# Kernel optimization log

Measured on AMD Instinct MI355X. Metric: run time of the kernel, lower is better.

The kernel has to match this reference:

```python
import jax, jax.numpy as jnp
import numpy as np
from jax import lax

DN = ('NCHW', 'OIHW', 'NCHW')

def conv(x, w, b, stride):
    y = lax.conv_general_dilated(x, w, (stride, stride), ((1, 1), (1, 1)), dimension_numbers=DN)
    return y + b[None, :, None, None]

def deconv(x, w, b):
    # PyTorch ConvTranspose2d(k=3, stride=2, padding=1, output_padding=1): doubles H, W.
    # w has torch layout [in, out, kH, kW]; convert to OIHW and flip spatially.
    wt = jnp.flip(w, (-2, -1)).transpose(1, 0, 2, 3)
    y = lax.conv_general_dilated(x, wt, (1, 1), ((1, 2), (1, 2)), lhs_dilation=(2, 2), dimension_numbers=DN)
    return y + b[None, :, None, None]


def setup_inputs() -> dict:
    key = jax.random.key(0)
    ks = jax.random.split(key, 16)
    s = 0.05
    d = {
        'x': jax.random.normal(ks[0], (16, 3, 256, 256), jnp.float32),
        'w1': jax.random.normal(ks[1], (64, 3, 3, 3), jnp.float32) * s,
        'b1': jnp.zeros((64,), jnp.float32),
        'w2': jax.random.normal(ks[2], (128, 64, 3, 3), jnp.float32) * s,
        'b2': jnp.zeros((128,), jnp.float32),
        'w3': jax.random.normal(ks[3], (256, 128, 3, 3), jnp.float32) * s,
        'b3': jnp.zeros((256,), jnp.float32),
        'w4': jax.random.normal(ks[4], (512, 256, 3, 3), jnp.float32) * s,
        'b4': jnp.zeros((512,), jnp.float32),
        'codebook': jax.random.normal(ks[5], (8192, 512), jnp.float32),
        # ConvTranspose2d weights in torch layout [in, out, kH, kW]
        'd1w': jax.random.normal(ks[6], (512, 256, 3, 3), jnp.float32) * s,
        'd1b': jnp.zeros((256,), jnp.float32),
        'd2w': jax.random.normal(ks[7], (256, 128, 3, 3), jnp.float32) * s,
        'd2b': jnp.zeros((128,), jnp.float32),
        'd3w': jax.random.normal(ks[8], (128, 64, 3, 3), jnp.float32) * s,
        'd3b': jnp.zeros((64,), jnp.float32),
        'wo': jax.random.normal(ks[9], (3, 64, 3, 3), jnp.float32) * s,
        'bo': jnp.zeros((3,), jnp.float32),
    }
    return d


def reference(x, w1, b1, w2, b2, w3, b3, w4, b4, codebook, d1w, d1b, d2w, d2b, d3w, d3b, wo, bo):
    # Encoder: 256 -> 256 -> 128 -> 64 -> 32 spatial
    h = jax.nn.relu(conv(x, w1, b1, 1))
    h = jax.nn.relu(conv(h, w2, b2, 2))
    h = jax.nn.relu(conv(h, w3, b3, 2))
    z = conv(h, w4, b4, 2)  # [B, 512, 32, 32]

    # Quantize: nearest codebook entry per spatial vector (channels-last).
    B, C, H, W = z.shape
    zf = z.transpose(0, 2, 3, 1).reshape(-1, C)  # [N, 512]
    # squared euclidean distances; argmin identical to cdist argmin
    d2 = (jnp.sum(zf * zf, axis=-1, keepdims=True)
          - 2.0 * (zf @ codebook.T)
          + jnp.sum(codebook * codebook, axis=-1))  # [N, K]
    indices = jnp.argmin(d2, axis=-1)  # [N]
    zq = codebook[indices].reshape(B, H, W, C).transpose(0, 3, 1, 2)  # [B, 512, 32, 32]

    # Decoder: 32 -> 64 -> 128 -> 256
    g = jax.nn.relu(deconv(zq, d1w, d1b))
    g = jax.nn.relu(deconv(g, d2w, d2b))
    g = jax.nn.relu(deconv(g, d3w, d3b))
    x_recon = jax.nn.sigmoid(conv(g, wo, bo, 1))
    return x_recon, indices
```

## Files before the change

kernel.cpp:

```cpp
#include <hip/hip_runtime.h>
#include <cstddef>

typedef short short8 __attribute__((ext_vector_type(8)));
typedef _Float16 half8 __attribute__((ext_vector_type(8)));
typedef _Float16 half4 __attribute__((ext_vector_type(4)));
typedef _Float16 half2v __attribute__((ext_vector_type(2)));
typedef float floatx4 __attribute__((ext_vector_type(4)));

__device__ __forceinline__ unsigned short f2bf(float f) {
    unsigned u = __float_as_uint(f);
    u += 0x7FFFu + ((u >> 16) & 1u);
    return (unsigned short)(u >> 16);
}
__device__ __forceinline__ float bf2f(unsigned short h) {
    return __uint_as_float((unsigned)h << 16);
}

__global__ __launch_bounds__(256)
void fused_conv12_mfma_kernel(const float* __restrict__ x,
                              const float* __restrict__ w1,
                              const float* __restrict__ b1,
                              const _Float16* __restrict__ w2h,
                              const _Float16* __restrict__ w2l,
                              const float* __restrict__ b2,
                              _Float16* __restrict__ outH,
                              _Float16* __restrict__ outL)
{
    __shared__ float s_x[3][11][36];
    __shared__ _Float16 sE[2][9][17][40];
    __shared__ _Float16 sO[2][9][16][40];

    const int tid = threadIdx.x;
    const int lane = tid & 63;
    const int wave = tid >> 6;
    const int n16 = lane & 15;
    const int quad = lane >> 4;

    const int ox0 = (blockIdx.x & 7) * 16;
    const int oy0 = (blockIdx.x >> 3) * 4;
    const int co0 = blockIdx.y * 64 + wave * 16;
    const int img = blockIdx.z;

    const int hy0 = oy0 * 2 - 1, hx0 = ox0 * 2 - 1;
    const int gy0 = hy0 - 1,     gx0 = hx0 - 1;
    const float* xN = x + (size_t)img * 3 * 65536;

    for (int e = tid; e < 3 * 11 * 35; e += 256) {
        int c = e / 385, r = e % 385;
        int yy = r / 35, xx = r % 35;
        int gy = gy0 + yy, gx = gx0 + xx;
        float v = 0.f;
        if ((unsigned)gy < 256u && (unsigned)gx < 256u)
            v = xN[(size_t)c * 65536 + gy * 256 + gx];
        s_x[c][yy][xx] = v;
    }

    floatx4 acc1[4], acc2[4];
#pragma unroll
    for (int s = 0; s < 4; s++) {
        acc1[s] = (floatx4){0.f, 0.f, 0.f, 0.f};
        acc2[s] = (floatx4){0.f, 0.f, 0.f, 0.f};
    }

    const int pair = tid & 15;
    const int pxg  = tid >> 4;

    for (int c0 = 0; c0 < 64; c0 += 32) {
        __syncthreads();

        const int ch0 = c0 + pair * 2;
        float wA[27], wB[27];
#pragma unroll
        for (int k = 0; k < 27; k++) {
            wA[k] = w1[ch0 * 27 + k];
            wB[k] = w1[ch0 * 27 + 27 + k];
        }
        const float bA = b1[ch0], bB = b1[ch0 + 1];

        for (int px = pxg; px < 33; px += 16) {
            const bool colok = (unsigned)(hx0 + px) < 256u;
            float xw[3][3][3];
#pragma unroll
            for (int c = 0; c < 3; c++)
#pragma unroll
                for (int r = 0; r < 3; r++)
#pragma unroll
                    for (int kx = 0; kx < 3; kx++)
                        xw[c][r][kx] = s_x[c][r][px + kx];
#pragma unroll
            for (int py = 0; py < 9; py++) {
                const bool inb = colok && (unsigned)(hy0 + py) < 256u;
                float aA = bA, aB = bB;
#pragma unroll
                for (int c = 0; c < 3; c++)
#pragma unroll
                    for (int k = 0; k < 9; k++) {
                        const float xv = xw[c][k / 3][k % 3];
                        aA += wA[c * 9 + k] * xv;
                        aB += wB[c * 9 + k] * xv;
                    }
                float vA = inb ? fmaxf(aA, 0.f) : 0.f;
                float vB = inb ? fmaxf(aB, 0.f) : 0.f;
                half2v hv, lv;
                _Float16 hA = (_Float16)vA, hB = (_Float16)vB;
                hv[0] = hA; hv[1] = hB;
                lv[0] = (_Float16)((vA - (float)hA) * 1024.f);
                lv[1] = (_Float16)((vB - (float)hB) * 1024.f);
                _Float16* dH = (px & 1) ? &sO[0][py][px >> 1][pair * 2]
                                        : &sE[0][py][px >> 1][pair * 2];
                _Float16* dL = (px & 1) ? &sO[1][py][px >> 1][pair * 2]
                                        : &sE[1][py][px >> 1][pair * 2];
                *(half2v*)dH = hv;
                *(half2v*)dL = lv;
                if (py < 8) {
#pragma unroll
                    for (int c = 0; c < 3; c++) {
#pragma unroll
                        for (int r = 0; r < 2; r++)
#pragma unroll
                            for (int kx = 0; kx < 3; kx++)
                                xw[c][r][kx] = xw[c][r + 1][kx];
#pragma unroll
                        for (int kx = 0; kx < 3; kx++)
                            xw[c][2][kx] = s_x[c][py + 3][px + kx];
                    }
                }
            }
        }
        __syncthreads();

        half8 ah[9], al[9];
#pragma unroll
        for (int tp = 0; tp < 9; tp++) {
            size_t o = ((size_t)(tp * 128 + co0 + n16)) * 64 + c0 + quad * 8;
            ah[tp] = *(const half8*)(w2h + o);
            al[tp] = *(const half8*)(w2l + o);
        }
#pragma unroll
        for (int oy = 0; oy < 4; oy++) {
#pragma unroll
            for (int tp = 0; tp < 9; tp++) {
                const int kx = tp % 3;
                const int row = oy * 2 + tp / 3;
                half8 bh, bl;
                if (kx == 0)      { bh = *(const half8*)&sE[0][row][n16][quad * 8];
                                    bl = *(const half8*)&sE[1][row][n16][quad * 8]; }
                else if (kx == 1) { bh = *(const half8*)&sO[0][row][n16][quad * 8];
                                    bl = *(const half8*)&sO[1][row][n16][quad * 8]; }
                else              { bh = *(const half8*)&sE[0][row][n16 + 1][quad * 8];
                                    bl = *(const half8*)&sE[1][row][n16 + 1][quad * 8]; }
                acc1[oy] = __builtin_amdgcn_mfma_f32_16x16x32_f16(ah[tp], bh, acc1[oy], 0, 0, 0);
                acc2[oy] = __builtin_amdgcn_mfma_f32_16x16x32_f16(ah[tp], bl, acc2[oy], 0, 0, 0);
                acc2[oy] = __builtin_amdgcn_mfma_f32_16x16x32_f16(al[tp], bh, acc2[oy], 0, 0, 0);
            }
        }
    }

    const float4 bv = *(const float4*)&b2[co0 + quad * 4];
    const float bb[4] = {bv.x, bv.y, bv.z, bv.w};
#pragma unroll
    for (int oy = 0; oy < 4; oy++) {
        half4 hv, lv;
#pragma unroll
        for (int r = 0; r < 4; r++) {
            float v = fmaxf(acc1[oy][r] + acc2[oy][r] * (1.0f / 1024.0f) + bb[r], 0.f);
            _Float16 h = (_Float16)v;
            hv[r] = h;
            lv[r] = (_Float16)((v - (float)h) * 1024.f);
        }
        size_t o = (((size_t)img * 128 + (oy0 + oy)) * 128 + (ox0 + n16)) * 128
                   + co0 + quad * 4;
        *(half4*)(outH + o) = hv;
        *(half4*)(outL + o) = lv;
    }
}

template<int CI, int CO>
__global__ __launch_bounds__(256)
void prepack_conv_kernel(const float* __restrict__ w,
                         _Float16* __restrict__ wh, _Float16* __restrict__ wl)
{
    int i = blockIdx.x * 256 + threadIdx.x;
    if (i >= CO * CI * 9) return;
    int co = i / (CI * 9);
    int r  = i % (CI * 9);
    int ci = r / 9;
    int tp = r % 9;
    float v = w[i];
    _Float16 h = (_Float16)v;
    size_t o = ((size_t)tp * CO + co) * CI + ci;
    wh[o] = h;
    wl[o] = (_Float16)((v - (float)h) * 1024.f);
}

template<int CIN, int COUT, int IH, int IW, bool RELU>
__global__ __launch_bounds__(256)
void conv_mfma_kernel(const _Float16* __restrict__ inH, const _Float16* __restrict__ inL,
                      const _Float16* __restrict__ wpH, const _Float16* __restrict__ wpL,
                      const float* __restrict__ bias,
                      _Float16* __restrict__ outH, _Float16* __restrict__ outL)
{
    constexpr int OH = IH / 2, OW = IW / 2;
    __shared__ _Float16 sE[2][9][17][40];
    __shared__ _Float16 sO[2][9][16][40];

    const int tid = threadIdx.x;
    const int lane = tid & 63;
    const int wave = tid >> 6;
    const int n16 = lane & 15;
    const int quad = lane >> 4;

    constexpr int NTX = OW / 16;
    const int ox0 = (blockIdx.x % NTX) * 16;
    const int oy0 = (blockIdx.x / NTX) * 4;
    const int co0 = blockIdx.y * 64 + wave * 16;
    const int img = blockIdx.z;

    const int iy0 = oy0 * 2 - 1;
    const int ix0 = ox0 * 2 - 1;
    const _Float16* iNH = inH + (size_t)img * IH * IW * CIN;
    const _Float16* iNL = inL + (size_t)img * IH * IW * CIN;

    floatx4 acc1[4], acc2[4];
#pragma unroll
    for (int s = 0; s < 4; s++) {
        acc1[s] = (floatx4){0.f, 0.f, 0.f, 0.f};
        acc2[s] = (floatx4){0.f, 0.f, 0.f, 0.f};
    }

    for (int k0 = 0; k0 < CIN; k0 += 32) {
        __syncthreads();
        for (int e = tid; e < 2376; e += 256) {
            int pl = e / 1188;
            int r  = e % 1188;
            int pix = r >> 2, q = r & 3;
            int py = pix / 33, px = pix % 33;
            int iy = iy0 + py, ix = ix0 + px;
            half8 v = (half8)(_Float16)0;
            if ((unsigned)iy < (unsigned)IH && (unsigned)ix < (unsigned)IW)
                v = *(const half8*)((pl ? iNL : iNH) + ((size_t)(iy * IW + ix) * CIN + k0 + q * 8));
            if (px & 1) *(half8*)&sO[pl][py][px >> 1][q * 8] = v;
            else        *(half8*)&sE[pl][py][px >> 1][q * 8] = v;
        }
        __syncthreads();

        half8 ah[9], al[9];
#pragma unroll
        for (int tp = 0; tp < 9; tp++) {
            size_t o = ((size_t)(tp * COUT + co0 + n16)) * CIN + k0 + quad * 8;
            ah[tp] = *(const half8*)(wpH + o);
            al[tp] = *(const half8*)(wpL + o);
        }

#pragma unroll
        for (int oy = 0; oy < 4; oy++) {
#pragma unroll
            for (int tp = 0; tp < 9; tp++) {
                const int ky = tp / 3, kx = tp % 3;
                const int row = oy * 2 + ky;
                half8 bh, bl;
                if (kx == 0)      { bh = *(const half8*)&sE[0][row][n16][quad * 8];
                                    bl = *(const half8*)&sE[1][row][n16][quad * 8]; }
                else if (kx == 1) { bh = *(const half8*)&sO[0][row][n16][quad * 8];
                                    bl = *(const half8*)&sO[1][row][n16][quad * 8]; }
                else              { bh = *(const half8*)&sE[0][row][n16 + 1][quad * 8];
                                    bl = *(const half8*)&sE[1][row][n16 + 1][quad * 8]; }
                acc1[oy] = __builtin_amdgcn_mfma_f32_16x16x32_f16(ah[tp], bh, acc1[oy], 0, 0, 0);
                acc2[oy] = __builtin_amdgcn_mfma_f32_16x16x32_f16(ah[tp], bl, acc2[oy], 0, 0, 0);
                acc2[oy] = __builtin_amdgcn_mfma_f32_16x16x32_f16(al[tp], bh, acc2[oy], 0, 0, 0);
            }
        }
    }

    const float4 bv = *(const float4*)&bias[co0 + quad * 4];
    const float bb[4] = {bv.x, bv.y, bv.z, bv.w};
#pragma unroll
    for (int oy = 0; oy < 4; oy++) {
        half4 hv, lv;
#pragma unroll
        for (int r = 0; r < 4; r++) {
            float v = acc1[oy][r] + acc2[oy][r] * (1.0f / 1024.0f) + bb[r];
            if (RELU) v = fmaxf(v, 0.f);
            _Float16 h = (_Float16)v;
            hv[r] = h;
            lv[r] = (_Float16)((v - (float)h) * 1024.f);
        }
        size_t o = (((size_t)img * OH + (oy0 + oy)) * OW + (ox0 + n16)) * COUT
                   + co0 + quad * 4;
        *(half4*)(outH + o) = hv;
        *(half4*)(outL + o) = lv;
    }
}

__global__ __launch_bounds__(64)
void cnorm_kernel(const float* __restrict__ cb, float* __restrict__ cn)
{
    const int code = blockIdx.x;
    const int t = threadIdx.x;
    const float* row = cb + (size_t)code * 512;
    float s = 0.f;
    for (int i = t; i < 512; i += 64) s += row[i] * row[i];
#pragma unroll
    for (int off = 32; off > 0; off >>= 1) s += __shfl_down(s, off, 64);
    if (t == 0) cn[code] = s;
}

__global__ __launch_bounds__(256)
void init_keys_kernel(unsigned long long* __restrict__ keys)
{
    keys[blockIdx.x * 256 + threadIdx.x] = ~0ull;
}

__global__ __launch_bounds__(256)
void split_cb_kernel(const float* __restrict__ cb,
                     _Float16* __restrict__ ch, _Float16* __restrict__ cl)
{
    size_t i = (size_t)blockIdx.x * 256 + threadIdx.x;
    float v = cb[i];
    _Float16 h = (_Float16)v;
    ch[i] = h;
    cl[i] = (_Float16)((v - (float)h) * 1024.f);
}

__global__ __launch_bounds__(256)
void vq_mfma_kernel(const _Float16* __restrict__ zh, const _Float16* __restrict__ zl,
                    const _Float16* __restrict__ ch, const _Float16* __restrict__ cl,
                    const float* __restrict__ cn,
                    unsigned long long* __restrict__ keys)
{
    __shared__ _Float16 sB[2][2][128][40];

    const int tid = threadIdx.x;
    const int lane = tid & 63;
    const int wave = tid >> 6;
    const int n16 = lane & 15;
    const int quad = lane >> 4;

    const int row0 = blockIdx.x * 128 + wave * 32;
    const int code0 = blockIdx.y * 128;

    floatx4 acc1[2][8], acc2[2][8];
#pragma unroll
    for (int rt = 0; rt < 2; rt++)
#pragma unroll
        for (int ct = 0; ct < 8; ct++) {
            acc1[rt][ct] = (floatx4){0.f, 0.f, 0.f, 0.f};
            acc2[rt][ct] = (floatx4){0.f, 0.f, 0.f, 0.f};
        }

    const _Float16* pzh = zh + (size_t)(row0 + n16) * 512 + quad * 8;
    const _Float16* pzl = zl + (size_t)(row0 + n16) * 512 + quad * 8;

    half8 As[2][4];
    As[0][0] = *(const half8*)(pzh);
    As[0][1] = *(const half8*)(pzh + 8192);
    As[0][2] = *(const half8*)(pzl);
    As[0][3] = *(const half8*)(pzl + 8192);
#pragma unroll
    for (int it = 0; it < 4; ++it) {
        int e = tid + it * 256;
        int pl = e >> 9, r = (e >> 2) & 127, q = e & 3;
        const _Float16* src = (pl ? cl : ch) + (size_t)(code0 + r) * 512 + q * 8;
        *(half8*)&sB[0][pl][r][q * 8] = *(const half8*)src;
    }
    __syncthreads();

#pragma unroll 2
    for (int c = 0; c < 16; ++c) {
        const int cur = c & 1;
        if (c < 15) {
            const int nxt = cur ^ 1;
            const int kk = (c + 1) * 32;
            As[nxt][0] = *(const half8*)(pzh + kk);
            As[nxt][1] = *(const half8*)(pzh + 8192 + kk);
            As[nxt][2] = *(const half8*)(pzl + kk);
            As[nxt][3] = *(const half8*)(pzl + 8192 + kk);
#pragma unroll
            for (int it = 0; it < 4; ++it) {
                int e = tid + it * 256;
                int pl = e >> 9, r = (e >> 2) & 127, q = e & 3;
                const _Float16* src = (pl ? cl : ch) + (size_t)(code0 + r) * 512 + kk + q * 8;
                *(half8*)&sB[nxt][pl][r][q * 8] = *(const half8*)src;
            }
        }
#pragma unroll
        for (int ct = 0; ct < 8; ++ct) {
            half8 bh = *(const half8*)&sB[cur][0][ct * 16 + n16][quad * 8];
            half8 bl = *(const half8*)&sB[cur][1][ct * 16 + n16][quad * 8];
            acc1[0][ct] = __builtin_amdgcn_mfma_f32_16x16x32_f16(As[cur][0], bh, acc1[0][ct], 0, 0, 0);
            acc1[1][ct] = __builtin_amdgcn_mfma_f32_16x16x32_f16(As[cur][1], bh, acc1[1][ct], 0, 0, 0);
            acc2[0][ct] = __builtin_amdgcn_mfma_f32_16x16x32_f16(As[cur][0], bl, acc2[0][ct], 0, 0, 0);
            acc2[1][ct] = __builtin_amdgcn_mfma_f32_16x16x32_f16(As[cur][1], bl, acc2[1][ct], 0, 0, 0);
            acc2[0][ct] = __builtin_amdgcn_mfma_f32_16x16x32_f16(As[cur][2], bh, acc2[0][ct], 0, 0, 0);
            acc2[1][ct] = __builtin_amdgcn_mfma_f32_16x16x32_f16(As[cur][3], bh, acc2[1][ct], 0, 0, 0);
        }
        __syncthreads();
    }

#pragma unroll
    for (int rt = 0; rt < 2; rt++) {
#pragma unroll
        for (int reg = 0; reg < 4; reg++) {
            float best = 3.0e38f;
            int bcode = 0;
#pragma unroll
            for (int ct = 0; ct < 8; ct++) {
                const int code = code0 + ct * 16 + n16;
                float dot = acc1[rt][ct][reg] + acc2[rt][ct][reg] * (1.0f / 1024.0f);
                float s = cn[code] - 2.0f * dot;
                if (s < best) { best = s; bcode = code; }
            }
            unsigned u = __float_as_uint(best);
            u = (u & 0x80000000u) ? ~u : (u | 0x80000000u);
            unsigned long long key = ((unsigned long long)u << 32) | (unsigned)bcode;
#pragma unroll
            for (int m = 1; m < 16; m <<= 1) {
                unsigned long long o = __shfl_xor(key, m, 64);
                key = (o < key) ? o : key;
            }
            if (n16 == 0)
                atomicMin(&keys[row0 + rt * 16 + quad * 4 + reg], key);
        }
    }
}

__global__ __launch_bounds__(256)
void vq_gather_kernel(const unsigned long long* __restrict__ keys,
                      const float* __restrict__ cb,
                      unsigned short* __restrict__ zq, float* __restrict__ idx_out)
{
    __shared__ int sidx[64];
    const int t = threadIdx.x;
    const int v0 = blockIdx.x * 64;
    if (t < 64) {
        int idx = (int)(keys[v0 + t] & 0xFFFFFFFFull);
        sidx[t] = idx;
        idx_out[v0 + t] = (float)idx;
    }
    __syncthreads();
    const int tv = t >> 2;
    const int q = t & 3;
    const float* crow = cb + (size_t)sidx[tv] * 512;
    unsigned short* zrow = zq + (size_t)(v0 + tv) * 512;
    for (int c = q * 8; c < 512; c += 32) {
        float4 f0 = *(const float4*)(crow + c);
        float4 f1 = *(const float4*)(crow + c + 4);
        short8 h;
        h[0] = (short)f2bf(f0.x); h[1] = (short)f2bf(f0.y);
        h[2] = (short)f2bf(f0.z); h[3] = (short)f2bf(f0.w);
        h[4] = (short)f2bf(f1.x); h[5] = (short)f2bf(f1.y);
        h[6] = (short)f2bf(f1.z); h[7] = (short)f2bf(f1.w);
        *(short8*)(zrow + c) = h;
    }
}

template<int CI, int CO>
__global__ __launch_bounds__(256)
void prepack_kernel(const float* __restrict__ w, unsigned short* __restrict__ wp)
{
    int i = blockIdx.x * 256 + threadIdx.x;
    if (i >= 9 * CO * CI) return;
    int ci = i / (CO * 9);
    int r  = i % (CO * 9);
    int co = r / 9;
    int tp = r % 9;
    wp[((size_t)tp * CO + co) * CI + ci] = f2bf(w[i]);
}

template<int CIN, int COUT, int IH, int IW, bool OUT_NCHW>
__global__ __launch_bounds__(256)
void deconv_mfma_kernel(const unsigned short* __restrict__ in,
                        const unsigned short* __restrict__ wp,
                        const float* __restrict__ bias,
                        unsigned short* __restrict__ out)
{
    constexpr int OH = 2 * IH, OW = 2 * IW;
    __shared__ short sIn[5][17][40];

    const int tid = threadIdx.x;
    const int lane = tid & 63;
    const int wave = tid >> 6;
    const int n16 = lane & 15;
    const int quad = lane >> 4;

    constexpr int NTX = IW / 16;
    const int x0 = (blockIdx.x % NTX) * 16;
    const int y0 = (blockIdx.x / NTX) * 4;
    const int co0 = blockIdx.y * 64 + wave * 16;
    const int img = blockIdx.z;

    const unsigned short* inN = in + (size_t)img * IH * IW * CIN;

    floatx4 acc[4][4];
#pragma unroll
    for (int s = 0; s < 4; s++)
#pragma unroll
        for (int c = 0; c < 4; c++) acc[s][c] = (floatx4){0.f, 0.f, 0.f, 0.f};

    for (int k0 = 0; k0 < CIN; k0 += 32) {
        __syncthreads();
        for (int e = tid; e < 340; e += 256) {
            int yy = e / 68, r = e % 68;
            int xx = r >> 2, q4 = r & 3;
            int gy = y0 + yy, gx = x0 + xx;
            short8 v = {0, 0, 0, 0, 0, 0, 0, 0};
            if (gy < IH && gx < IW)
                v = *(const short8*)(inN + ((size_t)(gy * IW + gx) * CIN + k0 + q4 * 8));
            *(short8*)&sIn[yy][xx][q4 * 8] = v;
        }
        __syncthreads();

        short8 a[9];
#pragma unroll
        for (int tp = 0; tp < 9; tp++)
            a[tp] = *(const short8*)(wp + ((size_t)(tp * COUT + co0 + n16) * CIN + k0 + quad * 8));

#pragma unroll
        for (int s = 0; s < 4; s++) {
            short8 b00 = *(const short8*)&sIn[s    ][n16    ][quad * 8];
            short8 b01 = *(const short8*)&sIn[s    ][n16 + 1][quad * 8];
            short8 b10 = *(const short8*)&sIn[s + 1][n16    ][quad * 8];
            short8 b11 = *(const short8*)&sIn[s + 1][n16 + 1][quad * 8];
            acc[s][0] = __builtin_amdgcn_mfma_f32_16x16x32_bf16(a[4], b00, acc[s][0], 0, 0, 0);
            acc[s][1] = __builtin_amdgcn_mfma_f32_16x16x32_bf16(a[3], b01, acc[s][1], 0, 0, 0);
            acc[s][1] = __builtin_amdgcn_mfma_f32_16x16x32_bf16(a[5], b00, acc[s][1], 0, 0, 0);
            acc[s][2] = __builtin_amdgcn_mfma_f32_16x16x32_bf16(a[1], b10, acc[s][2], 0, 0, 0);
            acc[s][2] = __builtin_amdgcn_mfma_f32_16x16x32_bf16(a[7], b00, acc[s][2], 0, 0, 0);
            acc[s][3] = __builtin_amdgcn_mfma_f32_16x16x32_bf16(a[0], b11, acc[s][3], 0, 0, 0);
            acc[s][3] = __builtin_amdgcn_mfma_f32_16x16x32_bf16(a[2], b10, acc[s][3], 0, 0, 0);
            acc[s][3] = __builtin_amdgcn_mfma_f32_16x16x32_bf16(a[6], b01, acc[s][3], 0, 0, 0);
            acc[s][3] = __builtin_amdgcn_mfma_f32_16x16x32_bf16(a[8], b00, acc[s][3], 0, 0, 0);
        }
    }

    const float4 bv = *(const float4*)&bias[co0 + quad * 4];
    const float bb[4] = {bv.x, bv.y, bv.z, bv.w};
    const int x = x0 + n16;

    if (!OUT_NCHW) {
        unsigned short* outN = out + (size_t)img * OH * OW * COUT;
#pragma unroll
        for (int s = 0; s < 4; s++) {
            const int y = y0 + s;
#pragma unroll
            for (int c = 0; c < 4; c++) {
                const int oy = 2 * y + (c >> 1);
                const int ox = 2 * x + (c & 1);
                ushort4 h;
                h.x = f2bf(fmaxf(acc[s][c][0] + bb[0], 0.f));
                h.y = f2bf(fmaxf(acc[s][c][1] + bb[1], 0.f));
                h.z = f2bf(fmaxf(acc[s][c][2] + bb[2], 0.f));
                h.w = f2bf(fmaxf(acc[s][c][3] + bb[3], 0.f));
                *(ushort4*)(outN + ((size_t)(oy * OW + ox) * COUT + co0 + quad * 4)) = h;
            }
        }
    } else {
#pragma unroll
        for (int s = 0; s < 4; s++) {
            const int y = y0 + s;
#pragma unroll
            for (int r = 0; r < 4; r++) {
                const int co = co0 + quad * 4 + r;
                unsigned short* oC = out + (size_t)(img * COUT + co) * OH * OW;
                unsigned p0 = (unsigned)f2bf(fmaxf(acc[s][0][r] + bb[r], 0.f)) |
                              ((unsigned)f2bf(fmaxf(acc[s][1][r] + bb[r], 0.f)) << 16);
                unsigned p1 = (unsigned)f2bf(fmaxf(acc[s][2][r] + bb[r], 0.f)) |
                              ((unsigned)f2bf(fmaxf(acc[s][3][r] + bb[r], 0.f)) << 16);
                *(unsigned*)(oC + (size_t)(2 * y) * OW + 2 * x) = p0;
                *(unsigned*)(oC + (size_t)(2 * y + 1) * OW + 2 * x) = p1;
            }
        }
    }
}

__global__ __launch_bounds__(256)
void conv_out_kernel(const unsigned short* __restrict__ in,
                     const float* __restrict__ w,
                     const float* __restrict__ bias,
                     float* __restrict__ out)
{
    constexpr int TIC = 4;
    __shared__ float s_in[TIC][3][258];
    const int t = threadIdx.x;
    const int y = blockIdx.x;
    const int n = blockIdx.y;
    const unsigned short* inN = in + (size_t)n * 64 * 65536;
    float acc0 = bias[0], acc1 = bias[1], acc2 = bias[2];

    for (int c0 = 0; c0 < 64; c0 += TIC) {
        for (int e = t; e < TIC * 3 * 258; e += 256) {
            int ci = e / 774;
            int r  = e % 774;
            int ry = r / 258, xx = r % 258;
            int gy = y - 1 + ry, gx = xx - 1;
            float v = 0.f;
            if ((unsigned)gy < 256u && (unsigned)gx < 256u)
                v = bf2f(inN[(size_t)(c0 + ci) * 65536 + gy * 256 + gx]);
            s_in[ci][ry][xx] = v;
        }
        __syncthreads();
#pragma unroll
        for (int ci = 0; ci < TIC; ++ci) {
            float iv[3][3];
#pragma unroll
            for (int ry = 0; ry < 3; ry++)
#pragma unroll
                for (int kx = 0; kx < 3; kx++)
                    iv[ry][kx] = s_in[ci][ry][t + kx];
#pragma unroll
            for (int k = 0; k < 9; k++) {
                const float v = iv[k / 3][k % 3];
                acc0 += w[(0 * 64 + c0 + ci) * 9 + k] * v;
                acc1 += w[(1 * 64 + c0 + ci) * 9 + k] * v;
                acc2 += w[(2 * 64 + c0 + ci) * 9 + k] * v;
            }
        }
        __syncthreads();
    }
    const size_t o = (size_t)((n * 3 + 0) * 256 + y) * 256 + t;
    out[o]          = 1.f / (1.f + __expf(-acc0));
    out[o + 65536]  = 1.f / (1.f + __expf(-acc1));
    out[o + 131072] = 1.f / (1.f + __expf(-acc2));
}

extern "C" void kernel_launch(void* const* d_in, const int* in_sizes, int n_in,
                              void* d_out, int out_size, void* d_ws, size_t ws_size,
                              hipStream_t stream)
{
    const float* x   = (const float*)d_in[0];
    const float* w1  = (const float*)d_in[1];
    const float* b1  = (const float*)d_in[2];
    const float* w2  = (const float*)d_in[3];
    const float* b2  = (const float*)d_in[4];
    const float* w3  = (const float*)d_in[5];
    const float* b3  = (const float*)d_in[6];
    const float* w4  = (const float*)d_in[7];
    const float* b4  = (const float*)d_in[8];
    const float* cb  = (const float*)d_in[9];
    const float* d1w = (const float*)d_in[10];
    const float* d1b = (const float*)d_in[11];
    const float* d2w = (const float*)d_in[12];
    const float* d2b = (const float*)d_in[13];
    const float* d3w = (const float*)d_in[14];
    const float* d3b = (const float*)d_in[15];
    const float* wo  = (const float*)d_in[16];
    const float* bo  = (const float*)d_in[17];

    char* ws = (char*)d_ws;
    _Float16* H2H = (_Float16*)(ws);
    _Float16* H2L = (_Float16*)(ws + 67108864);
    _Float16* H3H = (_Float16*)(ws + 134217728);
    _Float16* H3L = (_Float16*)(ws + 167772160);
    _Float16* ZH  = (_Float16*)(ws);
    _Float16* ZL  = (_Float16*)(ws + 16777216);
    unsigned short* ZQ = (unsigned short*)(ws + 33554432);
    _Float16* CBH = (_Float16*)(ws + 50331648);
    _Float16* CBL = (_Float16*)(ws + 58720256);
    unsigned short* G1 = (unsigned short*)(ws + 67108864);
    unsigned short* G2 = (unsigned short*)(ws + 134217728);
    unsigned short* G3 = (unsigned short*)(ws);
    unsigned long long* keys = (unsigned long long*)(ws + 201326592);
    float* cn = (float*)(ws + 201326592 + 131072);

    char* oscratch = (char*)d_out;
    _Float16* EW3H = (_Float16*)(oscratch);
    _Float16* EW3L = (_Float16*)(oscratch + 589824);
    _Float16* EW4H = (_Float16*)(oscratch + 1179648);
    _Float16* EW4L = (_Float16*)(oscratch + 3538944);
    unsigned short* WP1 = (unsigned short*)(oscratch + 5898240);
    unsigned short* WP2 = (unsigned short*)(oscratch + 8257536);
    unsigned short* WP3 = (unsigned short*)(oscratch + 8847360);
    _Float16* EW2H = (_Float16*)(oscratch + 8994816);
    _Float16* EW2L = (_Float16*)(oscratch + 9142272);

    float* xrec = (float*)d_out;
    float* idxf = (float*)d_out + (size_t)16 * 3 * 256 * 256;

    prepack_conv_kernel<64,  128><<<288,  256, 0, stream>>>(w2, EW2H, EW2L);
    prepack_conv_kernel<128, 256><<<1152, 256, 0, stream>>>(w3, EW3H, EW3L);
    prepack_conv_kernel<256, 512><<<4608, 256, 0, stream>>>(w4, EW4H, EW4L);
    prepack_kernel<512, 256><<<4608, 256, 0, stream>>>(d1w, WP1);
    prepack_kernel<256, 128><<<1152, 256, 0, stream>>>(d2w, WP2);
    prepack_kernel<128, 64 ><<<288,  256, 0, stream>>>(d3w, WP3);

    fused_conv12_mfma_kernel<<<dim3(256, 2, 16), 256, 0, stream>>>(x, w1, b1, EW2H, EW2L, b2, H2H, H2L);
    conv_mfma_kernel<128, 256, 128, 128, true ><<<dim3(64, 4, 16), 256, 0, stream>>>(H2H, H2L, EW3H, EW3L, b3, H3H, H3L);
    conv_mfma_kernel<256, 512, 64,  64,  false><<<dim3(16, 8, 16), 256, 0, stream>>>(H3H, H3L, EW4H, EW4L, b4, ZH, ZL);

    cnorm_kernel<<<8192, 64, 0, stream>>>(cb, cn);
    init_keys_kernel<<<64, 256, 0, stream>>>(keys);
    split_cb_kernel<<<16384, 256, 0, stream>>>(cb, CBH, CBL);
    vq_mfma_kernel<<<dim3(128, 64), 256, 0, stream>>>(ZH, ZL, CBH, CBL, cn, keys);
    vq_gather_kernel<<<256, 256, 0, stream>>>(keys, cb, ZQ, idxf);

    deconv_mfma_kernel<512, 256, 32,  32,  false><<<dim3(16,  4, 16), 256, 0, stream>>>(ZQ, WP1, d1b, G1);
    deconv_mfma_kernel<256, 128, 64,  64,  false><<<dim3(64,  2, 16), 256, 0, stream>>>(G1, WP2, d2b, G2);
    deconv_mfma_kernel<128, 64,  128, 128, true ><<<dim3(256, 1, 16), 256, 0, stream>>>(G2, WP3, d3b, G3);
    conv_out_kernel<<<dim3(256, 16), 256, 0, stream>>>(G3, wo, bo, xrec);
}
```

Before: 2.332 ms.

## Retile VQ distance kernel to 256 rows x 64 codes per block

Changes the VQ MFMA kernel tiling from 128 rows x 128 codes to 256 rows x 64 codes per block, with each wave computing a 64x64 tile (4x4 MFMA tiles). The codebook tile in shared memory is laid out linearly so each lane's fragment is contiguous, dropping the padded 2D layout. Next-chunk codebook loads are issued into registers before the MFMAs and stored to shared memory afterwards, giving a register-staged prefetch. The intent is better reuse of the loaded codebook fragments and fewer shared-memory reads per MFMA. The grid mapping changes (blockIdx.x now indexes codes), so the launch site must match, and the linear layout may cause LDS bank conflicts.

```diff
diff --git a/kernel.cpp b/kernel.cpp
--- a/kernel.cpp
+++ b/kernel.cpp
@@ -328,7 +328,7 @@
                     const float* __restrict__ cn,
                     unsigned long long* __restrict__ keys)
 {
-    __shared__ _Float16 sB[2][2][128][40];
+    __shared__ _Float16 sB[2][512 * 8];
 
     const int tid = threadIdx.x;
     const int lane = tid & 63;
@@ -336,14 +336,14 @@
     const int n16 = lane & 15;
     const int quad = lane >> 4;
 
-    const int row0 = blockIdx.x * 128 + wave * 32;
-    const int code0 = blockIdx.y * 128;
-
-    floatx4 acc1[2][8], acc2[2][8];
-#pragma unroll
-    for (int rt = 0; rt < 2; rt++)
-#pragma unroll
-        for (int ct = 0; ct < 8; ct++) {
+    const int code0 = blockIdx.x * 64;
+    const int row0 = blockIdx.y * 256 + wave * 64;
+
+    floatx4 acc1[4][4], acc2[4][4];
+#pragma unroll
+    for (int rt = 0; rt < 4; rt++)
+#pragma unroll
+        for (int ct = 0; ct < 4; ct++) {
             acc1[rt][ct] = (floatx4){0.f, 0.f, 0.f, 0.f};
             acc2[rt][ct] = (floatx4){0.f, 0.f, 0.f, 0.f};
         }
@@ -351,60 +351,57 @@
     const _Float16* pzh = zh + (size_t)(row0 + n16) * 512 + quad * 8;
     const _Float16* pzl = zl + (size_t)(row0 + n16) * 512 + quad * 8;
 
-    half8 As[2][4];
-    As[0][0] = *(const half8*)(pzh);
-    As[0][1] = *(const half8*)(pzh + 8192);
-    As[0][2] = *(const half8*)(pzl);
-    As[0][3] = *(const half8*)(pzl + 8192);
-#pragma unroll
-    for (int it = 0; it < 4; ++it) {
-        int e = tid + it * 256;
-        int pl = e >> 9, r = (e >> 2) & 127, q = e & 3;
-        const _Float16* src = (pl ? cl : ch) + (size_t)(code0 + r) * 512 + q * 8;
-        *(half8*)&sB[0][pl][r][q * 8] = *(const half8*)src;
-    }
+    const int e0 = tid, e1 = tid + 256;
+    const _Float16* s0 = ((e0 >> 8) ? cl : ch)
+        + (size_t)(code0 + ((e0 >> 6) & 3) * 16 + ((e0 >> 2) & 15)) * 512 + (e0 & 3) * 8;
+    const _Float16* s1 = ((e1 >> 8) ? cl : ch)
+        + (size_t)(code0 + ((e1 >> 6) & 3) * 16 + ((e1 >> 2) & 15)) * 512 + (e1 & 3) * 8;
+
+    *(half8*)&sB[0][e0 * 8] = *(const half8*)s0;
+    *(half8*)&sB[0][e1 * 8] = *(const half8*)s1;
     __syncthreads();
 
-#pragma unroll 2
     for (int c = 0; c < 16; ++c) {
         const int cur = c & 1;
+        const int kk = c * 32;
+        half8 ah[4], al[4];
+#pragma unroll
+        for (int rt = 0; rt < 4; rt++) {
+            ah[rt] = *(const half8*)(pzh + (size_t)rt * 8192 + kk);
+            al[rt] = *(const half8*)(pzl + (size_t)rt * 8192 + kk);
+        }
+        half8 t0, t1;
+        if (c < 15) {
+            t0 = *(const half8*)(s0 + kk + 32);
+            t1 = *(const half8*)(s1 + kk + 32);
+        }
+#pragma unroll
+        for (int ct = 0; ct < 4; ++ct) {
+            half8 bh = *(const half8*)&sB[cur][(ct * 64 + n16 * 4 + quad) * 8];
+            half8 bl = *(const half8*)&sB[cur][(256 + ct * 64 + n16 * 4 + quad) * 8];
+#pragma unroll
+            for (int rt = 0; rt < 4; rt++) {
+                acc1[rt][ct] = __builtin_amdgcn_mfma_f32_16x16x32_f16(ah[rt], bh, acc1[rt][ct], 0, 0, 0);
+                acc2[rt][ct] = __builtin_amdgcn_mfma_f32_16x16x32_f16(ah[rt], bl, acc2[rt][ct], 0, 0, 0);
+                acc2[rt][ct] = __builtin_amdgcn_mfma_f32_16x16x32_f16(al[rt], bh, acc2[rt][ct], 0, 0, 0);
+            }
+        }
         if (c < 15) {
             const int nxt = cur ^ 1;
-            const int kk = (c + 1) * 32;
-            As[nxt][0] = *(const half8*)(pzh + kk);
-            As[nxt][1] = *(const half8*)(pzh + 8192 + kk);
-            As[nxt][2] = *(const half8*)(pzl + kk);
-            As[nxt][3] = *(const half8*)(pzl + 8192 + kk);
-#pragma unroll
-            for (int it = 0; it < 4; ++it) {
-                int e = tid + it * 256;
-                int pl = e >> 9, r = (e >> 2) & 127, q = e & 3;
-                const _Float16* src = (pl ? cl : ch) + (size_t)(code0 + r) * 512 + kk + q * 8;
-                *(half8*)&sB[nxt][pl][r][q * 8] = *(const half8*)src;
-            }
-        }
-#pragma unroll
-        for (int ct = 0; ct < 8; ++ct) {
-            half8 bh = *(const half8*)&sB[cur][0][ct * 16 + n16][quad * 8];
-            half8 bl = *(const half8*)&sB[cur][1][ct * 16 + n16][quad * 8];
-            acc1[0][ct] = __builtin_amdgcn_mfma_f32_16x16x32_f16(As[cur][0], bh, acc1[0][ct], 0, 0, 0);
-            acc1[1][ct] = __builtin_amdgcn_mfma_f32_16x16x32_f16(As[cur][1], bh, acc1[1][ct], 0, 0, 0);
-            acc2[0][ct] = __builtin_amdgcn_mfma_f32_16x16x32_f16(As[cur][0], bl, acc2[0][ct], 0, 0, 0);
-            acc2[1][ct] = __builtin_amdgcn_mfma_f32_16x16x32_f16(As[cur][1], bl, acc2[1][ct], 0, 0, 0);
-            acc2[0][ct] = __builtin_amdgcn_mfma_f32_16x16x32_f16(As[cur][2], bh, acc2[0][ct], 0, 0, 0);
-            acc2[1][ct] = __builtin_amdgcn_mfma_f32_16x16x32_f16(As[cur][3], bh, acc2[1][ct], 0, 0, 0);
-        }
-        __syncthreads();
-    }
-
-#pragma unroll
-    for (int rt = 0; rt < 2; rt++) {
+            *(half8*)&sB[nxt][e0 * 8] = t0;
+            *(half8*)&sB[nxt][e1 * 8] = t1;
+        }
+        __syncthreads();
+    }
+
+#pragma unroll
+    for (int rt = 0; rt < 4; rt++) {
 #pragma unroll
         for (int reg = 0; reg < 4; reg++) {
             float best = 3.0e38f;
             int bcode = 0;
 #pragma unroll
-            for (int ct = 0; ct < 8; ct++) {
+            for (int ct = 0; ct < 4; ct++) {
                 const int code = code0 + ct * 16 + n16;
                 float dot = acc1[rt][ct][reg] + acc2[rt][ct][reg] * (1.0f / 1024.0f);
                 float s = cn[code] - 2.0f * dot;
```

Result: slower. 2.666 ms (+14.3%).
